# Kernel optimization log

Hardware: AMD Instinct MI355X
Metric: run time of the kernel (lower is better)

Reference implementation:

```python
import jax, jax.numpy as jnp
import numpy as np

N, D_IN = 8192, 256
L1_DIMS = [256, 128, 64]   # linear_list1
GNN_DIMS = [64, 64]        # gnn_list
L2_DIMS = [64, 32]         # linear_list2


def leaky(x):
    return jnp.where(x >= 0, x, 0.1 * x)


def _lin_params(key, din, dout, scale=0.05):
    k1, k2 = jax.random.split(key)
    W = jax.random.normal(k1, (dout, din), dtype=jnp.float32) * scale
    b = jax.random.normal(k2, (dout,), dtype=jnp.float32) * scale
    return W, b


def setup_inputs() -> dict:
    key = jax.random.key(0)
    ks = jax.random.split(key, 8)
    x = jax.random.normal(ks[0], (N, D_IN), dtype=jnp.float32)
    A = jax.random.uniform(ks[1], (N, N), dtype=jnp.float32)
    W1_0, b1_0 = _lin_params(ks[2], L1_DIMS[0], L1_DIMS[1])
    W1_1, b1_1 = _lin_params(ks[3], L1_DIMS[1], L1_DIMS[2])
    a = jax.random.normal(ks[4], (L1_DIMS[-1],), dtype=jnp.float32)
    Wg_0, bg_0 = _lin_params(ks[5], GNN_DIMS[0], GNN_DIMS[1])
    W2_0, b2_0 = _lin_params(ks[6], L2_DIMS[0], L2_DIMS[1])
    return {"x": x, "A": A, "W1_0": W1_0, "b1_0": b1_0, "W1_1": W1_1,
            "b1_1": b1_1, "a": a, "Wg_0": Wg_0, "bg_0": bg_0,
            "W2_0": W2_0, "b2_0": b2_0}


def reference(x, A, W1_0, b1_0, W1_1, b1_1, a, Wg_0, bg_0, W2_0, b2_0):
    # MLP encoder (linear_list1) with leakyrelu(0.1)
    x = leaky(x @ W1_0.T + b1_0)
    x = leaky(x @ W1_1.T + b1_1)  # [N, 64]

    # GAT-style scores: (x_i - x_j) @ a == s_i - s_j with s = x @ a
    s = x @ a                               # [N]
    S = jnp.exp(leaky(s[:, None] - s[None, :])) * A  # [N, N]
    S = S / jnp.sum(S, axis=-1, keepdims=True)

    # L1 = mean_ij( mean_d (x_i - x_j)^2 * S_ij )
    D = x.shape[-1]
    sq = jnp.sum(x * x, axis=-1) / D        # [N]
    pair_mse = sq[:, None] + sq[None, :] - (2.0 / D) * (x @ x.T)  # [N, N]
    L1 = jnp.mean(pair_mse * S)
    L2 = jnp.mean(S * S)

    # GNN layer(s): x = leakyrelu(Linear(S @ x))
    x = leaky((S @ x) @ Wg_0.T + bg_0)

    # output head (linear_list2), no activation
    x = x @ W2_0.T + b2_0
    return (x, L1, L2)
```

## Files before the change

kernel.cpp:

```cpp
#include <hip/hip_runtime.h>
#include <hip/hip_bf16.h>
#include <cstddef>
#include <cstdint>

#define NROWS 8192
#define LOG2E 1.4426950408889634f

typedef __attribute__((ext_vector_type(8))) short bf16x8;
typedef __attribute__((ext_vector_type(4))) float f32x4;

#define EXP2(x) __builtin_amdgcn_exp2f(x)

__device__ __forceinline__ short f2bf(float f) {
  unsigned u = __float_as_uint(f);
  u += 0x7fffu + ((u >> 16) & 1u);
  return (short)(u >> 16);
}
__device__ __forceinline__ float leaky_f(float v) { return fmaxf(v, 0.1f * v); }

union BFPair { __hip_bfloat162 h; unsigned u; };
__device__ __forceinline__ unsigned pack2(float a, float b) {
  BFPair p;
  p.h = __float22bfloat162_rn(make_float2(a, b));
  return p.u;
}

__device__ __forceinline__ f32x4 ntload4(const float* p) {
  return __builtin_nontemporal_load((const f32x4*)p);
}

extern "C" __global__ void __launch_bounds__(256)
encoder_kernel(const float* __restrict__ x, const float* __restrict__ W10,
               const float* __restrict__ b10, const float* __restrict__ W11,
               const float* __restrict__ b11, const float* __restrict__ avec,
               float* __restrict__ x2, float* __restrict__ sarr,
               float* __restrict__ sqarr, short* __restrict__ x2bfT) {
  __shared__ float xr[4][256];
  __shared__ float h1[4][128];
  const int t = threadIdx.x;
  const int r0 = blockIdx.x * 4;
#pragma unroll
  for (int r = 0; r < 4; ++r) xr[r][t] = x[(size_t)(r0 + r) * 256 + t];
  __syncthreads();
  if (t < 128) {
    float acc[4];
    const float b = b10[t];
#pragma unroll
    for (int r = 0; r < 4; ++r) acc[r] = b;
    const float* wrow = W10 + t * 256;
    for (int c = 0; c < 256; c += 4) {
      const float4 wv = *(const float4*)(wrow + c);
#pragma unroll
      for (int r = 0; r < 4; ++r) {
        acc[r] = fmaf(wv.x, xr[r][c], acc[r]);
        acc[r] = fmaf(wv.y, xr[r][c + 1], acc[r]);
        acc[r] = fmaf(wv.z, xr[r][c + 2], acc[r]);
        acc[r] = fmaf(wv.w, xr[r][c + 3], acc[r]);
      }
    }
#pragma unroll
    for (int r = 0; r < 4; ++r) h1[r][t] = leaky_f(acc[r]);
  }
  __syncthreads();
  if (t < 64) {
    float acc[4];
    const float b = b11[t];
#pragma unroll
    for (int r = 0; r < 4; ++r) acc[r] = b;
    const float* wrow = W11 + t * 128;
    for (int c = 0; c < 128; c += 4) {
      const float4 wv = *(const float4*)(wrow + c);
#pragma unroll
      for (int r = 0; r < 4; ++r) {
        acc[r] = fmaf(wv.x, h1[r][c], acc[r]);
        acc[r] = fmaf(wv.y, h1[r][c + 1], acc[r]);
        acc[r] = fmaf(wv.z, h1[r][c + 2], acc[r]);
        acc[r] = fmaf(wv.w, h1[r][c + 3], acc[r]);
      }
    }
    const float av = avec[t];
#pragma unroll
    for (int r = 0; r < 4; ++r) {
      const float v = leaky_f(acc[r]);
      x2[(size_t)(r0 + r) * 64 + t] = v;
      x2bfT[(size_t)t * NROWS + r0 + r] = f2bf(v);
      float ps = v * av, pq = v * v;
#pragma unroll
      for (int off = 1; off < 64; off <<= 1) {
        ps += __shfl_xor(ps, off);
        pq += __shfl_xor(pq, off);
      }
      if (t == 0) {
        sarr[r0 + r] = ps * LOG2E;
        sqarr[r0 + r] = pq * (1.0f / 64.0f);
      }
    }
  }
}

extern "C" __global__ void __launch_bounds__(256)
prep_kernel(const short* __restrict__ x2bfT, const float* __restrict__ sqarr,
            short* __restrict__ Bfrag, short* __restrict__ Ext) {
  const int S = blockIdx.x;
  const int t = threadIdx.x;
  const int nf = t >> 6, l = t & 63;
  const int fr = l & 15, kg = l >> 4;
  const bf16x8 v = *(const bf16x8*)(x2bfT + (size_t)(nf * 16 + fr) * NROWS + S * 32 + kg * 8);
  *(bf16x8*)(Bfrag + ((size_t)S * 4 + nf) * 512 + l * 8) = v;
  if (nf == 0) {
    bf16x8 e;
    if (fr == 0) {
#pragma unroll
      for (int i = 0; i < 8; ++i) e[i] = (short)0x3F80;
    } else if (fr == 1) {
#pragma unroll
      for (int i = 0; i < 8; ++i) e[i] = f2bf(sqarr[S * 32 + kg * 8 + i]);
    } else {
#pragma unroll
      for (int i = 0; i < 8; ++i) e[i] = 0;
    }
    *(bf16x8*)(Ext + (size_t)S * 512 + l * 8) = e;
  }
}

extern "C" __global__ void __launch_bounds__(256, 4)
fused16_kernel(const float* __restrict__ A, const float* __restrict__ sarr,
               const short* __restrict__ Bfrag, const short* __restrict__ Ext,
               float* __restrict__ yp, float* __restrict__ rsp,
               float* __restrict__ ssp, float* __restrict__ wsp) {
  __shared__ __attribute__((aligned(16))) char fragbuf[4][8448];
  __shared__ __attribute__((aligned(16))) float sjbuf[1024];
  __shared__ float sibuf[64];

  const int t = threadIdx.x;
  const int l = t & 63;
  const int w = __builtin_amdgcn_readfirstlane(t >> 6);
  const int fr = l & 15, kg = l >> 4;
  const int bi = blockIdx.x & 127;
  const int js = blockIdx.x >> 7;
  const int i0 = bi * 64;
  const int jb = js * 1024;
  const int row0 = i0 + w * 16;

  for (int k = t; k < 1024; k += 256) sjbuf[k] = sarr[jb + k];
  if (t < 64) sibuf[t] = sarr[i0 + t];
  __syncthreads();

  char* myf = fragbuf[w];
  const int ebase = (l >> 3) * 1056 + (((l & 7) >> 1) * 16) * 16 + (l & 1) * 8;

  f32x4 acc0 = {0.f,0.f,0.f,0.f}, acc1 = {0.f,0.f,0.f,0.f};
  f32x4 acc2 = {0.f,0.f,0.f,0.f}, acc3 = {0.f,0.f,0.f,0.f};
  f32x4 acce = {0.f,0.f,0.f,0.f}, accd = {0.f,0.f,0.f,0.f};

#pragma unroll 1
  for (int ch = 0; ch < 4; ++ch) {
    const float* ap = A + (size_t)row0 * NROWS + jb + ch * 256 + l * 4;
    const f32x4 sjv = *(const f32x4*)(sjbuf + ch * 256 + l * 4);

#pragma unroll
    for (int h = 0; h < 2; ++h) {
      f32x4 av[8];
#pragma unroll
      for (int r = 0; r < 8; ++r) av[r] = ntload4(ap + (size_t)(h * 8 + r) * NROWS);
#pragma unroll
      for (int r = 0; r < 8; ++r) {
        const int row = h * 8 + r;
        const float sif = sibuf[w * 16 + row];
        const float d0 = sif - sjv[0], d1 = sif - sjv[1];
        const float d2 = sif - sjv[2], d3 = sif - sjv[3];
        const float e0 = EXP2(fmaxf(d0, 0.1f * d0)) * av[r][0];
        const float e1 = EXP2(fmaxf(d1, 0.1f * d1)) * av[r][1];
        const float e2 = EXP2(fmaxf(d2, 0.1f * d2)) * av[r][2];
        const float e3 = EXP2(fmaxf(d3, 0.1f * d3)) * av[r][3];
        uint2 pk;
        pk.x = pack2(e0, e1);
        pk.y = pack2(e2, e3);
        *(uint2*)(myf + ebase + row * 16) = pk;
      }
    }
    asm volatile("s_waitcnt lgkmcnt(0)" ::: "memory");
    __builtin_amdgcn_sched_barrier(0);

    const int Sg0 = (jb + ch * 256) >> 5;
#pragma unroll
    for (int s = 0; s < 8; ++s) {
      const bf16x8 ar = *(const bf16x8*)(myf + s * 1056 + l * 16);
      const short* bp = Bfrag + (size_t)(Sg0 + s) * 2048 + l * 8;
      const bf16x8 b0 = *(const bf16x8*)(bp);
      const bf16x8 b1 = *(const bf16x8*)(bp + 512);
      const bf16x8 b2 = *(const bf16x8*)(bp + 1024);
      const bf16x8 b3 = *(const bf16x8*)(bp + 1536);
      const bf16x8 ef = *(const bf16x8*)(Ext + (size_t)(Sg0 + s) * 512 + l * 8);
      acc0 = __builtin_amdgcn_mfma_f32_16x16x32_bf16(ar, b0, acc0, 0, 0, 0);
      acc1 = __builtin_amdgcn_mfma_f32_16x16x32_bf16(ar, b1, acc1, 0, 0, 0);
      acc2 = __builtin_amdgcn_mfma_f32_16x16x32_bf16(ar, b2, acc2, 0, 0, 0);
      acc3 = __builtin_amdgcn_mfma_f32_16x16x32_bf16(ar, b3, acc3, 0, 0, 0);
      acce = __builtin_amdgcn_mfma_f32_16x16x32_bf16(ar, ef, acce, 0, 0, 0);
      accd = __builtin_amdgcn_mfma_f32_16x16x32_bf16(ar, ar, accd, 0, 0, 0);
    }
    asm volatile("s_waitcnt lgkmcnt(0)" ::: "memory");
    __builtin_amdgcn_sched_barrier(0);
  }

  float* ypb = yp + (size_t)js * NROWS * 64;
  const f32x4 accs[4] = {acc0, acc1, acc2, acc3};
#pragma unroll
  for (int nf = 0; nf < 4; ++nf)
#pragma unroll
    for (int ri = 0; ri < 4; ++ri)
      ypb[(size_t)(row0 + kg * 4 + ri) * 64 + nf * 16 + fr] = accs[nf][ri];
#pragma unroll
  for (int ri = 0; ri < 4; ++ri) {
    const int gi = row0 + kg * 4 + ri;
    if (fr == 0) rsp[js * NROWS + gi] = acce[ri];
    if (fr == 1) wsp[js * NROWS + gi] = acce[ri];
    if (fr == kg * 4 + ri) ssp[js * NROWS + gi] = accd[ri];
  }
}

extern "C" __global__ void __launch_bounds__(256)
finish_kernel(const float* __restrict__ x2, const float* __restrict__ sqarr,
              const float* __restrict__ yp, const float* __restrict__ rsp,
              const float* __restrict__ ssp, const float* __restrict__ wsp,
              const float* __restrict__ Wg, const float* __restrict__ bg,
              const float* __restrict__ W2, const float* __restrict__ b2,
              float* __restrict__ outp, float* __restrict__ l1c, float* __restrict__ l2c) {
  __shared__ float hbuf[4][64];
  __shared__ float gbuf[4][64];
  const int t = threadIdx.x;
  const int w = t >> 6, lane = t & 63;
  const int i = blockIdx.x * 4 + w;

  float yv = 0.f, rowsum = 0.f, sumsq = 0.f, wsq = 0.f;
#pragma unroll
  for (int p = 0; p < 8; ++p) {
    yv += yp[(size_t)p * NROWS * 64 + (size_t)i * 64 + lane];
    rowsum += rsp[p * NROWS + i];
    sumsq += ssp[p * NROWS + i];
    wsq += wsp[p * NROWS + i];
  }
  const float inv = 1.0f / rowsum;
  hbuf[w][lane] = yv * inv;
  const float xv = x2[(size_t)i * 64 + lane];
  float xy = xv * yv;
#pragma unroll
  for (int off = 1; off < 64; off <<= 1) xy += __shfl_xor(xy, off);
  if (lane == 0) {
    l1c[i] = sqarr[i] + (wsq - (2.0f / 64.0f) * xy) * inv;
    l2c[i] = sumsq * inv * inv;
  }
  __syncthreads();
  float accg = bg[lane];
  {
    const float* wrow = Wg + lane * 64;
#pragma unroll 4
    for (int d = 0; d < 64; ++d) accg = fmaf(wrow[d], hbuf[w][d], accg);
  }
  gbuf[w][lane] = leaky_f(accg);
  __syncthreads();
  if (lane < 32) {
    float acco = b2[lane];
    const float* wrow = W2 + lane * 64;
#pragma unroll 4
    for (int d = 0; d < 64; ++d) acco = fmaf(wrow[d], gbuf[w][d], acco);
    outp[(size_t)i * 32 + lane] = acco;
  }
}

extern "C" __global__ void __launch_bounds__(256)
loss_kernel(const float* __restrict__ l1c, const float* __restrict__ l2c,
            float* __restrict__ outp) {
  __shared__ float s1[256], s2[256];
  const int t = threadIdx.x;
  float a1 = 0.f, a2 = 0.f;
  for (int i = t * 4; i < NROWS; i += 1024) {
    const float4 v1 = *(const float4*)(l1c + i);
    const float4 v2 = *(const float4*)(l2c + i);
    a1 += (v1.x + v1.y) + (v1.z + v1.w);
    a2 += (v2.x + v2.y) + (v2.z + v2.w);
  }
  s1[t] = a1; s2[t] = a2;
  __syncthreads();
  for (int off = 128; off > 0; off >>= 1) {
    if (t < off) { s1[t] += s1[t + off]; s2[t] += s2[t + off]; }
    __syncthreads();
  }
  if (t == 0) {
    const float scale = 1.0f / ((float)NROWS * (float)NROWS);
    outp[NROWS * 32] = s1[0] * scale;
    outp[NROWS * 32 + 1] = s2[0] * scale;
  }
}

extern "C" void kernel_launch(void* const* d_in, const int* in_sizes, int n_in,
                              void* d_out, int out_size, void* d_ws, size_t ws_size,
                              hipStream_t stream) {
  const float* x   = (const float*)d_in[0];
  const float* A   = (const float*)d_in[1];
  const float* W10 = (const float*)d_in[2];
  const float* b10 = (const float*)d_in[3];
  const float* W11 = (const float*)d_in[4];
  const float* b11 = (const float*)d_in[5];
  const float* av  = (const float*)d_in[6];
  const float* Wg  = (const float*)d_in[7];
  const float* bg  = (const float*)d_in[8];
  const float* W2  = (const float*)d_in[9];
  const float* b2  = (const float*)d_in[10];
  float* out = (float*)d_out;

  float* ws    = (float*)d_ws;
  float* x2    = ws;
  float* sarr  = x2 + (size_t)NROWS * 64;
  float* sqarr = sarr + NROWS;
  float* l1c   = sqarr + NROWS;
  float* l2c   = l1c + NROWS;
  float* rsp   = l2c + NROWS;
  float* ssp   = rsp + (size_t)8 * NROWS;
  float* wsp   = ssp + (size_t)8 * NROWS;
  float* yp    = wsp + (size_t)8 * NROWS;
  short* x2bfT = (short*)(yp + (size_t)8 * NROWS * 64);
  short* Bfrag = x2bfT + (size_t)NROWS * 64;
  short* Ext   = Bfrag + (size_t)256 * 2048;

  hipLaunchKernelGGL(encoder_kernel, dim3(2048), dim3(256), 0, stream,
                     x, W10, b10, W11, b11, av, x2, sarr, sqarr, x2bfT);
  hipLaunchKernelGGL(prep_kernel, dim3(256), dim3(256), 0, stream,
                     x2bfT, sqarr, Bfrag, Ext);
  hipLaunchKernelGGL(fused16_kernel, dim3(1024), dim3(256), 0, stream,
                     A, sarr, Bfrag, Ext, yp, rsp, ssp, wsp);
  hipLaunchKernelGGL(finish_kernel, dim3(2048), dim3(256), 0, stream,
                     x2, sqarr, yp, rsp, ssp, wsp, Wg, bg, W2, b2, out, l1c, l2c);
  hipLaunchKernelGGL(loss_kernel, dim3(1), dim3(256), 0, stream, l1c, l2c, out);
}
```

Measured before the change: 187.1 us.

## Split fused score+GEMM into bf16 convert pass and separate MFMA GEMM

Replaces the fused kernel that computed exp-scores from A and fed them straight into MFMA with three kernels. A convert kernel writes bf16 scores to a workspace matrix along with per-chunk row sums, squared sums and sq-weighted sums. A rowreduce kernel folds those partials, and a standalone GEMM multiplies the bf16 matrix by x in 16 K-partitions. This frees the GEMM from the exp work and LDS staging, but adds a 128 MB bf16 write and reread plus extra launches, and doubles the partial-output reduction in finish.

```diff
diff --git a/kernel.cpp b/kernel.cpp
--- a/kernel.cpp
+++ b/kernel.cpp
@@ -24,7 +24,6 @@
   p.h = __float22bfloat162_rn(make_float2(a, b));
   return p.u;
 }
-
 __device__ __forceinline__ f32x4 ntload4(const float* p) {
   return __builtin_nontemporal_load((const f32x4*)p);
 }
@@ -99,130 +98,120 @@
 }
 
 extern "C" __global__ void __launch_bounds__(256)
-prep_kernel(const short* __restrict__ x2bfT, const float* __restrict__ sqarr,
-            short* __restrict__ Bfrag, short* __restrict__ Ext) {
+prep16_kernel(const short* __restrict__ x2bfT, short* __restrict__ Bfrag) {
   const int S = blockIdx.x;
   const int t = threadIdx.x;
   const int nf = t >> 6, l = t & 63;
+  const bf16x8 v = *(const bf16x8*)(x2bfT + (size_t)(nf * 16 + (l & 15)) * NROWS
+                                    + S * 32 + (l >> 4) * 8);
+  *(bf16x8*)(Bfrag + ((size_t)S * 4 + nf) * 512 + l * 8) = v;
+}
+
+extern "C" __global__ void __launch_bounds__(256)
+convert_kernel(const float* __restrict__ A, const float* __restrict__ sarr,
+               const float* __restrict__ sqarr, short* __restrict__ raw,
+               float* __restrict__ rspc, float* __restrict__ sspc,
+               float* __restrict__ wspc) {
+  const int t = threadIdx.x, l = t & 63, w = t >> 6;
+  const int gw = blockIdx.x * 4 + w;
+#pragma unroll 1
+  for (int k = 0; k < 32; ++k) {
+    const int chunk = gw + k * 8192;
+    const int i = chunk >> 5;
+    const int jc = (chunk & 31) << 8;
+    const float sif = sarr[i];
+    const f32x4 a4 = ntload4(A + (size_t)chunk * 256 + l * 4);
+    const f32x4 sj = *(const f32x4*)(sarr + jc + l * 4);
+    const f32x4 sq = *(const f32x4*)(sqarr + jc + l * 4);
+    const float d0 = sif - sj[0], d1 = sif - sj[1];
+    const float d2 = sif - sj[2], d3 = sif - sj[3];
+    const float r0 = EXP2(fmaxf(d0, 0.1f * d0)) * a4[0];
+    const float r1 = EXP2(fmaxf(d1, 0.1f * d1)) * a4[1];
+    const float r2 = EXP2(fmaxf(d2, 0.1f * d2)) * a4[2];
+    const float r3 = EXP2(fmaxf(d3, 0.1f * d3)) * a4[3];
+    uint2 pk;
+    pk.x = pack2(r0, r1);
+    pk.y = pack2(r2, r3);
+    *(uint2*)(raw + (size_t)chunk * 256 + l * 4) = pk;
+    float a = (r0 + r1) + (r2 + r3);
+    float b = fmaf(r0, r0, fmaf(r1, r1, fmaf(r2, r2, r3 * r3)));
+    float c = fmaf(r0, sq[0], fmaf(r1, sq[1], fmaf(r2, sq[2], r3 * sq[3])));
+#pragma unroll
+    for (int off = 1; off < 64; off <<= 1) {
+      a += __shfl_xor(a, off);
+      b += __shfl_xor(b, off);
+      c += __shfl_xor(c, off);
+    }
+    if (l == 0) { rspc[chunk] = a; sspc[chunk] = b; wspc[chunk] = c; }
+  }
+}
+
+extern "C" __global__ void __launch_bounds__(256)
+rowreduce_kernel(const float* __restrict__ rspc, const float* __restrict__ sspc,
+                 const float* __restrict__ wspc, float* __restrict__ rs,
+                 float* __restrict__ ss, float* __restrict__ ws) {
+  const int i = blockIdx.x * 256 + threadIdx.x;
+  float a = 0.f, b = 0.f, c = 0.f;
+#pragma unroll
+  for (int q = 0; q < 32; ++q) {
+    a += rspc[i * 32 + q];
+    b += sspc[i * 32 + q];
+    c += wspc[i * 32 + q];
+  }
+  rs[i] = a; ss[i] = b; ws[i] = c;
+}
+
+extern "C" __global__ void __launch_bounds__(256)
+gemm_kernel(const short* __restrict__ raw, const short* __restrict__ Bfrag,
+            float* __restrict__ yp) {
+  const int t = threadIdx.x, l = t & 63, w = t >> 6;
+  const int rtp = blockIdx.x >> 2;
+  const int kp = blockIdx.x & 3;
+  const int S0 = kp * 64 + w * 16;
+  const int row0 = rtp * 32;
+  const short* a0 = raw + (size_t)(row0 + (l & 15)) * NROWS + S0 * 32 + (l >> 4) * 8;
+  const short* a1 = a0 + (size_t)16 * NROWS;
+  const short* bp = Bfrag + (size_t)S0 * 2048 + l * 8;
+
+  f32x4 acc0[4], acc1[4];
+#pragma unroll
+  for (int nf = 0; nf < 4; ++nf) {
+    acc0[nf] = (f32x4){0.f, 0.f, 0.f, 0.f};
+    acc1[nf] = (f32x4){0.f, 0.f, 0.f, 0.f};
+  }
+#pragma unroll
+  for (int s = 0; s < 16; ++s) {
+    const bf16x8 ar0 = *(const bf16x8*)(a0 + s * 32);
+    const bf16x8 ar1 = *(const bf16x8*)(a1 + s * 32);
+    const short* bs = bp + (size_t)s * 2048;
+    const bf16x8 b0 = *(const bf16x8*)(bs);
+    const bf16x8 b1 = *(const bf16x8*)(bs + 512);
+    const bf16x8 b2 = *(const bf16x8*)(bs + 1024);
+    const bf16x8 b3 = *(const bf16x8*)(bs + 1536);
+    acc0[0] = __builtin_amdgcn_mfma_f32_16x16x32_bf16(ar0, b0, acc0[0], 0, 0, 0);
+    acc0[1] = __builtin_amdgcn_mfma_f32_16x16x32_bf16(ar0, b1, acc0[1], 0, 0, 0);
+    acc0[2] = __builtin_amdgcn_mfma_f32_16x16x32_bf16(ar0, b2, acc0[2], 0, 0, 0);
+    acc0[3] = __builtin_amdgcn_mfma_f32_16x16x32_bf16(ar0, b3, acc0[3], 0, 0, 0);
+    acc1[0] = __builtin_amdgcn_mfma_f32_16x16x32_bf16(ar1, b0, acc1[0], 0, 0, 0);
+    acc1[1] = __builtin_amdgcn_mfma_f32_16x16x32_bf16(ar1, b1, acc1[1], 0, 0, 0);
+    acc1[2] = __builtin_amdgcn_mfma_f32_16x16x32_bf16(ar1, b2, acc1[2], 0, 0, 0);
+    acc1[3] = __builtin_amdgcn_mfma_f32_16x16x32_bf16(ar1, b3, acc1[3], 0, 0, 0);
+  }
+  float* ypb = yp + (size_t)(kp * 4 + w) * NROWS * 64;
   const int fr = l & 15, kg = l >> 4;
-  const bf16x8 v = *(const bf16x8*)(x2bfT + (size_t)(nf * 16 + fr) * NROWS + S * 32 + kg * 8);
-  *(bf16x8*)(Bfrag + ((size_t)S * 4 + nf) * 512 + l * 8) = v;
-  if (nf == 0) {
-    bf16x8 e;
-    if (fr == 0) {
-#pragma unroll
-      for (int i = 0; i < 8; ++i) e[i] = (short)0x3F80;
-    } else if (fr == 1) {
-#pragma unroll
-      for (int i = 0; i < 8; ++i) e[i] = f2bf(sqarr[S * 32 + kg * 8 + i]);
-    } else {
-#pragma unroll
-      for (int i = 0; i < 8; ++i) e[i] = 0;
-    }
-    *(bf16x8*)(Ext + (size_t)S * 512 + l * 8) = e;
-  }
-}
-
-extern "C" __global__ void __launch_bounds__(256, 4)
-fused16_kernel(const float* __restrict__ A, const float* __restrict__ sarr,
-               const short* __restrict__ Bfrag, const short* __restrict__ Ext,
-               float* __restrict__ yp, float* __restrict__ rsp,
-               float* __restrict__ ssp, float* __restrict__ wsp) {
-  __shared__ __attribute__((aligned(16))) char fragbuf[4][8448];
-  __shared__ __attribute__((aligned(16))) float sjbuf[1024];
-  __shared__ float sibuf[64];
-
-  const int t = threadIdx.x;
-  const int l = t & 63;
-  const int w = __builtin_amdgcn_readfirstlane(t >> 6);
-  const int fr = l & 15, kg = l >> 4;
-  const int bi = blockIdx.x & 127;
-  const int js = blockIdx.x >> 7;
-  const int i0 = bi * 64;
-  const int jb = js * 1024;
-  const int row0 = i0 + w * 16;
-
-  for (int k = t; k < 1024; k += 256) sjbuf[k] = sarr[jb + k];
-  if (t < 64) sibuf[t] = sarr[i0 + t];
-  __syncthreads();
-
-  char* myf = fragbuf[w];
-  const int ebase = (l >> 3) * 1056 + (((l & 7) >> 1) * 16) * 16 + (l & 1) * 8;
-
-  f32x4 acc0 = {0.f,0.f,0.f,0.f}, acc1 = {0.f,0.f,0.f,0.f};
-  f32x4 acc2 = {0.f,0.f,0.f,0.f}, acc3 = {0.f,0.f,0.f,0.f};
-  f32x4 acce = {0.f,0.f,0.f,0.f}, accd = {0.f,0.f,0.f,0.f};
-
-#pragma unroll 1
-  for (int ch = 0; ch < 4; ++ch) {
-    const float* ap = A + (size_t)row0 * NROWS + jb + ch * 256 + l * 4;
-    const f32x4 sjv = *(const f32x4*)(sjbuf + ch * 256 + l * 4);
-
-#pragma unroll
-    for (int h = 0; h < 2; ++h) {
-      f32x4 av[8];
-#pragma unroll
-      for (int r = 0; r < 8; ++r) av[r] = ntload4(ap + (size_t)(h * 8 + r) * NROWS);
-#pragma unroll
-      for (int r = 0; r < 8; ++r) {
-        const int row = h * 8 + r;
-        const float sif = sibuf[w * 16 + row];
-        const float d0 = sif - sjv[0], d1 = sif - sjv[1];
-        const float d2 = sif - sjv[2], d3 = sif - sjv[3];
-        const float e0 = EXP2(fmaxf(d0, 0.1f * d0)) * av[r][0];
-        const float e1 = EXP2(fmaxf(d1, 0.1f * d1)) * av[r][1];
-        const float e2 = EXP2(fmaxf(d2, 0.1f * d2)) * av[r][2];
-        const float e3 = EXP2(fmaxf(d3, 0.1f * d3)) * av[r][3];
-        uint2 pk;
-        pk.x = pack2(e0, e1);
-        pk.y = pack2(e2, e3);
-        *(uint2*)(myf + ebase + row * 16) = pk;
-      }
-    }
-    asm volatile("s_waitcnt lgkmcnt(0)" ::: "memory");
-    __builtin_amdgcn_sched_barrier(0);
-
-    const int Sg0 = (jb + ch * 256) >> 5;
-#pragma unroll
-    for (int s = 0; s < 8; ++s) {
-      const bf16x8 ar = *(const bf16x8*)(myf + s * 1056 + l * 16);
-      const short* bp = Bfrag + (size_t)(Sg0 + s) * 2048 + l * 8;
-      const bf16x8 b0 = *(const bf16x8*)(bp);
-      const bf16x8 b1 = *(const bf16x8*)(bp + 512);
-      const bf16x8 b2 = *(const bf16x8*)(bp + 1024);
-      const bf16x8 b3 = *(const bf16x8*)(bp + 1536);
-      const bf16x8 ef = *(const bf16x8*)(Ext + (size_t)(Sg0 + s) * 512 + l * 8);
-      acc0 = __builtin_amdgcn_mfma_f32_16x16x32_bf16(ar, b0, acc0, 0, 0, 0);
-      acc1 = __builtin_amdgcn_mfma_f32_16x16x32_bf16(ar, b1, acc1, 0, 0, 0);
-      acc2 = __builtin_amdgcn_mfma_f32_16x16x32_bf16(ar, b2, acc2, 0, 0, 0);
-      acc3 = __builtin_amdgcn_mfma_f32_16x16x32_bf16(ar, b3, acc3, 0, 0, 0);
-      acce = __builtin_amdgcn_mfma_f32_16x16x32_bf16(ar, ef, acce, 0, 0, 0);
-      accd = __builtin_amdgcn_mfma_f32_16x16x32_bf16(ar, ar, accd, 0, 0, 0);
-    }
-    asm volatile("s_waitcnt lgkmcnt(0)" ::: "memory");
-    __builtin_amdgcn_sched_barrier(0);
-  }
-
-  float* ypb = yp + (size_t)js * NROWS * 64;
-  const f32x4 accs[4] = {acc0, acc1, acc2, acc3};
 #pragma unroll
   for (int nf = 0; nf < 4; ++nf)
 #pragma unroll
-    for (int ri = 0; ri < 4; ++ri)
-      ypb[(size_t)(row0 + kg * 4 + ri) * 64 + nf * 16 + fr] = accs[nf][ri];
-#pragma unroll
-  for (int ri = 0; ri < 4; ++ri) {
-    const int gi = row0 + kg * 4 + ri;
-    if (fr == 0) rsp[js * NROWS + gi] = acce[ri];
-    if (fr == 1) wsp[js * NROWS + gi] = acce[ri];
-    if (fr == kg * 4 + ri) ssp[js * NROWS + gi] = accd[ri];
-  }
+    for (int ri = 0; ri < 4; ++ri) {
+      ypb[(size_t)(row0 + kg * 4 + ri) * 64 + nf * 16 + fr] = acc0[nf][ri];
+      ypb[(size_t)(row0 + 16 + kg * 4 + ri) * 64 + nf * 16 + fr] = acc1[nf][ri];
+    }
 }
 
 extern "C" __global__ void __launch_bounds__(256)
 finish_kernel(const float* __restrict__ x2, const float* __restrict__ sqarr,
-              const float* __restrict__ yp, const float* __restrict__ rsp,
-              const float* __restrict__ ssp, const float* __restrict__ wsp,
+              const float* __restrict__ yp, const float* __restrict__ rs,
+              const float* __restrict__ ss, const float* __restrict__ ws,
               const float* __restrict__ Wg, const float* __restrict__ bg,
               const float* __restrict__ W2, const float* __restrict__ b2,
               float* __restrict__ outp, float* __restrict__ l1c, float* __restrict__ l2c) {
@@ -232,14 +221,11 @@
   const int w = t >> 6, lane = t & 63;
   const int i = blockIdx.x * 4 + w;
 
-  float yv = 0.f, rowsum = 0.f, sumsq = 0.f, wsq = 0.f;
-#pragma unroll
-  for (int p = 0; p < 8; ++p) {
+  float yv = 0.f;
+#pragma unroll
+  for (int p = 0; p < 16; ++p)
     yv += yp[(size_t)p * NROWS * 64 + (size_t)i * 64 + lane];
-    rowsum += rsp[p * NROWS + i];
-    sumsq += ssp[p * NROWS + i];
-    wsq += wsp[p * NROWS + i];
-  }
+  const float rowsum = rs[i], sumsq = ss[i], wsq = ws[i];
   const float inv = 1.0f / rowsum;
   hbuf[w][lane] = yv * inv;
   const float xv = x2[(size_t)i * 64 + lane];
@@ -309,27 +295,32 @@
   const float* b2  = (const float*)d_in[10];
   float* out = (float*)d_out;
 
-  float* ws    = (float*)d_ws;
-  float* x2    = ws;
+  float* ws_f  = (float*)d_ws;
+  float* x2    = ws_f;
   float* sarr  = x2 + (size_t)NROWS * 64;
   float* sqarr = sarr + NROWS;
   float* l1c   = sqarr + NROWS;
   float* l2c   = l1c + NROWS;
-  float* rsp   = l2c + NROWS;
-  float* ssp   = rsp + (size_t)8 * NROWS;
-  float* wsp   = ssp + (size_t)8 * NROWS;
-  float* yp    = wsp + (size_t)8 * NROWS;
-  short* x2bfT = (short*)(yp + (size_t)8 * NROWS * 64);
+  float* rs    = l2c + NROWS;
+  float* ssum  = rs + NROWS;
+  float* wsq   = ssum + NROWS;
+  float* rspc  = wsq + NROWS;
+  float* sspc  = rspc + 262144;
+  float* wspc  = sspc + 262144;
+  float* yp    = wspc + 262144;
+  short* x2bfT = (short*)(yp + (size_t)16 * NROWS * 64);
   short* Bfrag = x2bfT + (size_t)NROWS * 64;
-  short* Ext   = Bfrag + (size_t)256 * 2048;
+  short* raw   = Bfrag + (size_t)256 * 2048;
 
   hipLaunchKernelGGL(encoder_kernel, dim3(2048), dim3(256), 0, stream,
                      x, W10, b10, W11, b11, av, x2, sarr, sqarr, x2bfT);
-  hipLaunchKernelGGL(prep_kernel, dim3(256), dim3(256), 0, stream,
-                     x2bfT, sqarr, Bfrag, Ext);
-  hipLaunchKernelGGL(fused16_kernel, dim3(1024), dim3(256), 0, stream,
-                     A, sarr, Bfrag, Ext, yp, rsp, ssp, wsp);
+  hipLaunchKernelGGL(prep16_kernel, dim3(256), dim3(256), 0, stream, x2bfT, Bfrag);
+  hipLaunchKernelGGL(convert_kernel, dim3(2048), dim3(256), 0, stream,
+                     A, sarr, sqarr, raw, rspc, sspc, wspc);
+  hipLaunchKernelGGL(rowreduce_kernel, dim3(32), dim3(256), 0, stream,
+                     rspc, sspc, wspc, rs, ssum, wsq);
+  hipLaunchKernelGGL(gemm_kernel, dim3(1024), dim3(256), 0, stream, raw, Bfrag, yp);
   hipLaunchKernelGGL(finish_kernel, dim3(2048), dim3(256), 0, stream,
-                     x2, sqarr, yp, rsp, ssp, wsp, Wg, bg, W2, b2, out, l1c, l2c);
+                     x2, sqarr, yp, rs, ssum, wsq, Wg, bg, W2, b2, out, l1c, l2c);
   hipLaunchKernelGGL(loss_kernel, dim3(1), dim3(256), 0, stream, l1c, l2c, out);
 }
```

Measured after the change: 223.4 us. +19.4%, slower.
